# Optimization experiments

Hardware: AMD Instinct MI355X
Metric: run time of the kernel (lower is better)

Reference implementation:

```python
import jax, jax.numpy as jnp
import numpy as np

B, L, D, H = 2, 256, 256, 4
DH = D // H  # 64


def setup_inputs() -> dict:
    key = jax.random.key(0)
    ks = jax.random.split(key, 20)
    inp = {
        "q": jax.random.normal(ks[0], (B, L, D), jnp.float32),
        "k": jax.random.normal(ks[1], (B, L, D), jnp.float32),
        "v": jax.random.normal(ks[2], (B, L, D), jnp.float32),
        "attn_mask": jnp.zeros((L, L), jnp.float32),  # nonzero => masked
        "key_padding_mask": jnp.zeros((B, L), bool),
        "pitch_rel": jax.random.normal(ks[3], (B, L, L, D), jnp.float32),
        "dur_rel": jax.random.normal(ks[4], (B, L, L, D), jnp.float32),
    }
    scale = 1.0 / np.sqrt(D)
    names = ["Wq", "Wk", "Wv", "fc", "pr", "dr"]
    for i, n in enumerate(names):
        inp[n + "_w"] = jax.random.normal(ks[5 + 2 * i], (D, D), jnp.float32) * scale
        inp[n + "_b"] = jax.random.normal(ks[6 + 2 * i], (D,), jnp.float32) * 0.01
    return inp


def _linear(x, w, b):
    # torch nn.Linear: y = x @ W^T + b
    return jnp.matmul(x, w.T) + b


def reference(q, k, v, attn_mask, key_padding_mask, pitch_rel, dur_rel,
              Wq_w, Wq_b, Wk_w, Wk_b, Wv_w, Wv_b, fc_w, fc_b,
              pr_w, pr_b, dr_w, dr_b):
    Bq, Lq, Dm = q.shape
    Lk = k.shape[1]
    # project and split heads -> (B, H, L, DH)
    def heads(x, w, b):
        return _linear(x, w, b).reshape(Bq, -1, H, DH).transpose(0, 2, 1, 3)
    qh, kh, vh = heads(q, Wq_w, Wq_b), heads(k, Wk_w, Wk_b), heads(v, Wv_w, Wv_b)

    # content scores: (B, H, Lq, Lk)
    logits = jnp.einsum("bhid,bhjd->bhij", qh, kh)

    # relative pitch bias: pitch_rel (B, Lq, Lk, D) -> (B, Lq, Lk, H, DH)
    pr = _linear(pitch_rel, pr_w, pr_b).reshape(Bq, Lq, Lk, H, DH)
    logits = logits + jnp.einsum("bhid,bijhd->bhij", qh, pr)

    dr = _linear(dur_rel, dr_w, dr_b).reshape(Bq, Lq, Lk, H, DH)
    logits = logits + jnp.einsum("bhid,bijhd->bhij", qh, dr)

    logits = logits / np.sqrt(DH)

    # mask: key_padding_mask broadcast over the QUERY axis (as in source),
    # attn_mask nonzero => masked
    mask = jnp.logical_or(key_padding_mask[:, None, :, None],
                          (attn_mask != 0)[None, None, :, :])
    logits = jnp.where(mask, jnp.float32(-9e15), logits)

    attn = jax.nn.softmax(logits, axis=-1)  # (B, H, Lq, Lk)
    out = jnp.einsum("bhij,bhjd->bhid", attn, vh)  # (B, H, Lq, DH)
    out = out.transpose(0, 2, 1, 3).reshape(Bq, Lq, Dm)
    out = _linear(out, fc_w, fc_b)  # dropout is identity in eval mode
    return out, attn
```

## Files before the change

### kernel.cpp

```cpp
#include <hip/hip_runtime.h>
#include <math.h>


__global__ __launch_bounds__(256) void k_proj(
    const float* __restrict__ q, const float* __restrict__ k_, const float* __restrict__ v,
    const float* __restrict__ Wq, const float* __restrict__ Bq,
    const float* __restrict__ Wk, const float* __restrict__ Bk,
    const float* __restrict__ Wv, const float* __restrict__ Bv,
    float* __restrict__ qh, float* __restrict__ kh, float* __restrict__ vh) {
  int blk = blockIdx.x;
  int m = blk >> 5;
  int r = blk & 31;
  int b = r >> 4, it = (r >> 2) & 3, ot = r & 3;
  const float* X = (m == 0) ? q : (m == 1) ? k_ : v;
  const float* W = (m == 0) ? Wq : (m == 1) ? Wk : Wv;
  const float* Bs = (m == 0) ? Bq : (m == 1) ? Bk : Bv;
  float* OUT = (m == 0) ? qh : (m == 1) ? kh : vh;
  const float scale = (m == 0) ? 0.125f : 1.0f;

  __shared__ float xs[64][33];
  __shared__ float ws[64][33];
  int tid = threadIdx.x;
  int ti = tid >> 4, to = tid & 15;
  int lr = tid >> 2, lc = (tid & 3) * 8;
  float acc[4][4] = {};

  for (int k0 = 0; k0 < 256; k0 += 32) {
    float4 a0 = *(const float4*)(X + (size_t)(b * 256 + it * 64 + lr) * 256 + k0 + lc);
    float4 a1 = *(const float4*)(X + (size_t)(b * 256 + it * 64 + lr) * 256 + k0 + lc + 4);
    xs[lr][lc + 0] = a0.x; xs[lr][lc + 1] = a0.y; xs[lr][lc + 2] = a0.z; xs[lr][lc + 3] = a0.w;
    xs[lr][lc + 4] = a1.x; xs[lr][lc + 5] = a1.y; xs[lr][lc + 6] = a1.z; xs[lr][lc + 7] = a1.w;
    float4 w0 = *(const float4*)(W + (size_t)(ot * 64 + lr) * 256 + k0 + lc);
    float4 w1 = *(const float4*)(W + (size_t)(ot * 64 + lr) * 256 + k0 + lc + 4);
    ws[lr][lc + 0] = w0.x; ws[lr][lc + 1] = w0.y; ws[lr][lc + 2] = w0.z; ws[lr][lc + 3] = w0.w;
    ws[lr][lc + 4] = w1.x; ws[lr][lc + 5] = w1.y; ws[lr][lc + 6] = w1.z; ws[lr][lc + 7] = w1.w;
    __syncthreads();
#pragma unroll
    for (int kk = 0; kk < 32; ++kk) {
      float xv0 = xs[ti * 4 + 0][kk], xv1 = xs[ti * 4 + 1][kk];
      float xv2 = xs[ti * 4 + 2][kk], xv3 = xs[ti * 4 + 3][kk];
      float wv0 = ws[0 * 16 + to][kk], wv1 = ws[1 * 16 + to][kk];
      float wv2 = ws[2 * 16 + to][kk], wv3 = ws[3 * 16 + to][kk];
      acc[0][0] += xv0 * wv0; acc[0][1] += xv0 * wv1; acc[0][2] += xv0 * wv2; acc[0][3] += xv0 * wv3;
      acc[1][0] += xv1 * wv0; acc[1][1] += xv1 * wv1; acc[1][2] += xv1 * wv2; acc[1][3] += xv1 * wv3;
      acc[2][0] += xv2 * wv0; acc[2][1] += xv2 * wv1; acc[2][2] += xv2 * wv2; acc[2][3] += xv2 * wv3;
      acc[3][0] += xv3 * wv0; acc[3][1] += xv3 * wv1; acc[3][2] += xv3 * wv2; acc[3][3] += xv3 * wv3;
    }
    __syncthreads();
  }
#pragma unroll
  for (int ii = 0; ii < 4; ++ii)
#pragma unroll
    for (int oo = 0; oo < 4; ++oo) {
      int i = it * 64 + ti * 4 + ii;
      int dd = oo * 16 + to;
      OUT[(size_t)((b * 4 + ot) * 256 + i) * 64 + dd] = (acc[ii][oo] + Bs[ot * 64 + dd]) * scale;
    }
}

static __device__ void body_qprdr(int blk, const float* __restrict__ qh,
                                  const float* __restrict__ prw, const float* __restrict__ drw,
                                  float* __restrict__ qpr, float* __restrict__ qdr) {
  int t = blk >> 7;
  int r2 = blk & 127;
  int rt = r2 >> 2, et = r2 & 3;
  const float* W = t ? drw : prw;
  float* OUT = t ? qdr : qpr;
  int h = (rt >> 2) & 3;

  __shared__ float xs[64][33];
  __shared__ float ws2[32][64];
  int tid = threadIdx.x;
  int ti = tid >> 4, to = tid & 15;
  float acc[4][4] = {};

  for (int k0 = 0; k0 < 64; k0 += 32) {
    int lr = tid >> 2, lc = (tid & 3) * 8;
    float4 a0 = *(const float4*)(qh + (size_t)(rt * 64 + lr) * 64 + k0 + lc);
    float4 a1 = *(const float4*)(qh + (size_t)(rt * 64 + lr) * 64 + k0 + lc + 4);
    xs[lr][lc + 0] = a0.x; xs[lr][lc + 1] = a0.y; xs[lr][lc + 2] = a0.z; xs[lr][lc + 3] = a0.w;
    xs[lr][lc + 4] = a1.x; xs[lr][lc + 5] = a1.y; xs[lr][lc + 6] = a1.z; xs[lr][lc + 7] = a1.w;
    int wr = tid >> 3, wc = (tid & 7) * 8;
    float4 w0 = *(const float4*)(W + (size_t)(h * 64 + k0 + wr) * 256 + et * 64 + wc);
    float4 w1 = *(const float4*)(W + (size_t)(h * 64 + k0 + wr) * 256 + et * 64 + wc + 4);
    ws2[wr][wc + 0] = w0.x; ws2[wr][wc + 1] = w0.y; ws2[wr][wc + 2] = w0.z; ws2[wr][wc + 3] = w0.w;
    ws2[wr][wc + 4] = w1.x; ws2[wr][wc + 5] = w1.y; ws2[wr][wc + 6] = w1.z; ws2[wr][wc + 7] = w1.w;
    __syncthreads();
#pragma unroll
    for (int kk = 0; kk < 32; ++kk) {
      float xv0 = xs[ti * 4 + 0][kk], xv1 = xs[ti * 4 + 1][kk];
      float xv2 = xs[ti * 4 + 2][kk], xv3 = xs[ti * 4 + 3][kk];
      float wv0 = ws2[kk][0 * 16 + to], wv1 = ws2[kk][1 * 16 + to];
      float wv2 = ws2[kk][2 * 16 + to], wv3 = ws2[kk][3 * 16 + to];
      acc[0][0] += xv0 * wv0; acc[0][1] += xv0 * wv1; acc[0][2] += xv0 * wv2; acc[0][3] += xv0 * wv3;
      acc[1][0] += xv1 * wv0; acc[1][1] += xv1 * wv1; acc[1][2] += xv1 * wv2; acc[1][3] += xv1 * wv3;
      acc[2][0] += xv2 * wv0; acc[2][1] += xv2 * wv1; acc[2][2] += xv2 * wv2; acc[2][3] += xv2 * wv3;
      acc[3][0] += xv3 * wv0; acc[3][1] += xv3 * wv1; acc[3][2] += xv3 * wv2; acc[3][3] += xv3 * wv3;
    }
    __syncthreads();
  }
#pragma unroll
  for (int ii = 0; ii < 4; ++ii)
#pragma unroll
    for (int oo = 0; oo < 4; ++oo)
      OUT[(size_t)(rt * 64 + ti * 4 + ii) * 256 + et * 64 + oo * 16 + to] = acc[ii][oo];
}

static __device__ void body_qk(int blk, const float* __restrict__ qh,
                               const float* __restrict__ kh, float* __restrict__ qk) {
  int bh = blk >> 4, it = (blk >> 2) & 3, jt = blk & 3;
  __shared__ float xs[64][33];
  __shared__ float ys[64][33];
  int tid = threadIdx.x;
  int ti = tid >> 4, to = tid & 15;
  float acc[4][4] = {};

  for (int k0 = 0; k0 < 64; k0 += 32) {
    int lr = tid >> 2, lc = (tid & 3) * 8;
    float4 a0 = *(const float4*)(qh + (size_t)(bh * 256 + it * 64 + lr) * 64 + k0 + lc);
    float4 a1 = *(const float4*)(qh + (size_t)(bh * 256 + it * 64 + lr) * 64 + k0 + lc + 4);
    xs[lr][lc + 0] = a0.x; xs[lr][lc + 1] = a0.y; xs[lr][lc + 2] = a0.z; xs[lr][lc + 3] = a0.w;
    xs[lr][lc + 4] = a1.x; xs[lr][lc + 5] = a1.y; xs[lr][lc + 6] = a1.z; xs[lr][lc + 7] = a1.w;
    float4 b0 = *(const float4*)(kh + (size_t)(bh * 256 + jt * 64 + lr) * 64 + k0 + lc);
    float4 b1 = *(const float4*)(kh + (size_t)(bh * 256 + jt * 64 + lr) * 64 + k0 + lc + 4);
    ys[lr][lc + 0] = b0.x; ys[lr][lc + 1] = b0.y; ys[lr][lc + 2] = b0.z; ys[lr][lc + 3] = b0.w;
    ys[lr][lc + 4] = b1.x; ys[lr][lc + 5] = b1.y; ys[lr][lc + 6] = b1.z; ys[lr][lc + 7] = b1.w;
    __syncthreads();
#pragma unroll
    for (int kk = 0; kk < 32; ++kk) {
      float xv0 = xs[ti * 4 + 0][kk], xv1 = xs[ti * 4 + 1][kk];
      float xv2 = xs[ti * 4 + 2][kk], xv3 = xs[ti * 4 + 3][kk];
      float wv0 = ys[0 * 16 + to][kk], wv1 = ys[1 * 16 + to][kk];
      float wv2 = ys[2 * 16 + to][kk], wv3 = ys[3 * 16 + to][kk];
      acc[0][0] += xv0 * wv0; acc[0][1] += xv0 * wv1; acc[0][2] += xv0 * wv2; acc[0][3] += xv0 * wv3;
      acc[1][0] += xv1 * wv0; acc[1][1] += xv1 * wv1; acc[1][2] += xv1 * wv2; acc[1][3] += xv1 * wv3;
      acc[2][0] += xv2 * wv0; acc[2][1] += xv2 * wv1; acc[2][2] += xv2 * wv2; acc[2][3] += xv2 * wv3;
      acc[3][0] += xv3 * wv0; acc[3][1] += xv3 * wv1; acc[3][2] += xv3 * wv2; acc[3][3] += xv3 * wv3;
    }
    __syncthreads();
  }
#pragma unroll
  for (int ii = 0; ii < 4; ++ii)
#pragma unroll
    for (int jj = 0; jj < 4; ++jj)
      qk[(size_t)(bh * 256 + it * 64 + ti * 4 + ii) * 256 + jt * 64 + jj * 16 + to] = acc[ii][jj];
}

static __device__ void body_transpose(int blk, const float* __restrict__ in,
                                      float* __restrict__ out) {
  __shared__ float t[32][33];
  int bx = blk & 7, by = blk >> 3;
  int x = threadIdx.x & 31, y0 = threadIdx.x >> 5;
#pragma unroll
  for (int yy = 0; yy < 32; yy += 8)
    t[yy + y0][x] = in[(size_t)(by * 32 + yy + y0) * 256 + bx * 32 + x];
  __syncthreads();
#pragma unroll
  for (int yy = 0; yy < 32; yy += 8)
    out[(size_t)(bx * 32 + yy + y0) * 256 + by * 32 + x] = t[x][yy + y0];
}

__global__ __launch_bounds__(256) void k_mid(
    const float* __restrict__ qh, const float* __restrict__ kh,
    const float* __restrict__ prw, const float* __restrict__ drw,
    float* __restrict__ qpr, float* __restrict__ qdr, float* __restrict__ qk,
    const float* __restrict__ fcw, float* __restrict__ fcT) {
  int blk = blockIdx.x;
  if (blk < 256) body_qprdr(blk, qh, prw, drw, qpr, qdr);
  else if (blk < 384) body_qk(blk - 256, qh, kh, qk);
  else body_transpose(blk - 384, fcw, fcT);
}

__global__ __launch_bounds__(256, 8) void k_bias(
    const float* __restrict__ pitch, const float* __restrict__ dur,
    const float* __restrict__ qpr, const float* __restrict__ qdr,
    float* __restrict__ bias) {
  int blk = blockIdx.x;
  int jc = blk & 3;
  int bi = blk >> 2;
  int b = bi >> 8, i = bi & 255;
  int tid = threadIdx.x, w = tid >> 6, l = tid & 63;
  int j0 = jc * 64 + w * 16;

  __shared__ float red[4][4][4][65];

  float4 qp[4], qd[4];
#pragma unroll
  for (int h = 0; h < 4; ++h) {
    qp[h] = *(const float4*)(qpr + (size_t)((b * 4 + h) * 256 + i) * 256 + 4 * l);
    qd[h] = *(const float4*)(qdr + (size_t)((b * 4 + h) * 256 + i) * 256 + 4 * l);
  }

  int p2 = l & 15, row_o = p2 >> 2, h_o = p2 & 3, sub = l >> 4;
  size_t obase = ((size_t)(b * 4 + h_o) * 256 + i) * 256 + j0 + row_o;

  const float* pbase = pitch + ((size_t)bi * 256 + j0) * 256 + 4 * l;
  const float* dbase = dur + ((size_t)bi * 256 + j0) * 256 + 4 * l;

#pragma unroll
  for (int g = 0; g < 4; ++g) {
#pragma unroll
    for (int r = 0; r < 4; ++r) {
      float4 P = *(const float4*)(pbase + (g * 4 + r) * 256);
      float4 Dv = *(const float4*)(dbase + (g * 4 + r) * 256);
      red[w][r][0][l] = P.x * qp[0].x + P.y * qp[0].y + P.z * qp[0].z + P.w * qp[0].w
                      + Dv.x * qd[0].x + Dv.y * qd[0].y + Dv.z * qd[0].z + Dv.w * qd[0].w;
      red[w][r][1][l] = P.x * qp[1].x + P.y * qp[1].y + P.z * qp[1].z + P.w * qp[1].w
                      + Dv.x * qd[1].x + Dv.y * qd[1].y + Dv.z * qd[1].z + Dv.w * qd[1].w;
      red[w][r][2][l] = P.x * qp[2].x + P.y * qp[2].y + P.z * qp[2].z + P.w * qp[2].w
                      + Dv.x * qd[2].x + Dv.y * qd[2].y + Dv.z * qd[2].z + Dv.w * qd[2].w;
      red[w][r][3][l] = P.x * qp[3].x + P.y * qp[3].y + P.z * qp[3].z + P.w * qp[3].w
                      + Dv.x * qd[3].x + Dv.y * qd[3].y + Dv.z * qd[3].z + Dv.w * qd[3].w;
    }
    float x = 0.f;
    {
      const float* rr = &red[w][row_o][h_o][sub * 16];
#pragma unroll
      for (int c = 0; c < 16; ++c) x += rr[c];
    }
    x += __shfl_xor(x, 16);
    x += __shfl_xor(x, 32);
    if (l < 16) bias[obase + g * 4] = x;
  }
}

__global__ __launch_bounds__(256) void k_pvfc(
    const float* __restrict__ bias, const float* __restrict__ amask,
    const unsigned char* __restrict__ kpm, const float* __restrict__ vh,
    const float* __restrict__ fcT, const float* __restrict__ fcb,
    float* __restrict__ attn, float* __restrict__ out) {
  int b = blockIdx.x >> 8, i = blockIdx.x & 255;
  int tid = threadIdx.x;
  int h = tid >> 6, l = tid & 63;

  __shared__ float arow[4][256];
  __shared__ float pre[256];

  bool rowm = kpm[b * 256 + i] != 0;
  float* qrow = attn + (size_t)((b * 4 + h) * 256 + i) * 256;
  const float* brow = bias + (size_t)((b * 4 + h) * 256 + i) * 256;
  float4 v4 = *(float4*)(qrow + 4 * l);
  float4 b4 = *(const float4*)(brow + 4 * l);
  float4 m4 = *(const float4*)(amask + (size_t)i * 256 + 4 * l);
  float v0 = (rowm || m4.x != 0.f) ? -9e15f : v4.x + b4.x;
  float v1 = (rowm || m4.y != 0.f) ? -9e15f : v4.y + b4.y;
  float v2 = (rowm || m4.z != 0.f) ? -9e15f : v4.z + b4.z;
  float v3 = (rowm || m4.w != 0.f) ? -9e15f : v4.w + b4.w;

  float mx = fmaxf(fmaxf(v0, v1), fmaxf(v2, v3));
#pragma unroll
  for (int m = 1; m <= 32; m <<= 1) mx = fmaxf(mx, __shfl_xor(mx, m));
  float e0 = __expf(v0 - mx), e1 = __expf(v1 - mx);
  float e2 = __expf(v2 - mx), e3 = __expf(v3 - mx);
  float sm = e0 + e1 + e2 + e3;
#pragma unroll
  for (int m = 1; m <= 32; m <<= 1) sm += __shfl_xor(sm, m);
  float inv = 1.0f / sm;
  float4 a4 = make_float4(e0 * inv, e1 * inv, e2 * inv, e3 * inv);
  *(float4*)(qrow + 4 * l) = a4;
  *(float4*)&arow[h][4 * l] = a4;

  float acc = 0.f;
  const float* vbase = vh + (size_t)(b * 4 + h) * 256 * 64 + l;
#pragma unroll 4
  for (int jj = 0; jj < 256; ++jj) acc += arow[h][jj] * vbase[(size_t)jj * 64];
  pre[tid] = acc;
  __syncthreads();

  float acc2 = fcb[tid];
#pragma unroll 4
  for (int c = 0; c < 256; ++c) acc2 += pre[c] * fcT[(size_t)c * 256 + tid];
  out[(size_t)(b * 256 + i) * 256 + tid] = acc2;
}

extern "C" void kernel_launch(void* const* d_in, const int* in_sizes, int n_in,
                              void* d_out, int out_size, void* d_ws, size_t ws_size,
                              hipStream_t stream) {
  (void)in_sizes; (void)n_in; (void)out_size; (void)ws_size;
  const float* q = (const float*)d_in[0];
  const float* k = (const float*)d_in[1];
  const float* v = (const float*)d_in[2];
  const float* amask = (const float*)d_in[3];
  const unsigned char* kpm = (const unsigned char*)d_in[4];
  const float* pitch = (const float*)d_in[5];
  const float* dur = (const float*)d_in[6];
  const float* Wq = (const float*)d_in[7];
  const float* Bq = (const float*)d_in[8];
  const float* Wk = (const float*)d_in[9];
  const float* Bk = (const float*)d_in[10];
  const float* Wv = (const float*)d_in[11];
  const float* Bv = (const float*)d_in[12];
  const float* fcw = (const float*)d_in[13];
  const float* fcb = (const float*)d_in[14];
  const float* prw = (const float*)d_in[15];
  const float* drw = (const float*)d_in[17];

  float* out = (float*)d_out;
  float* attn = out + 2 * 256 * 256;

  float* wsf = (float*)d_ws;
  float* qh = wsf;
  float* kh = qh + 131072;
  float* vh = kh + 131072;
  float* qpr = vh + 131072;
  float* qdr = qpr + 524288;
  float* fcT = qdr + 524288;
  float* bias = fcT + 65536;

  k_proj<<<96, 256, 0, stream>>>(q, k, v, Wq, Bq, Wk, Bk, Wv, Bv, qh, kh, vh);
  k_mid<<<448, 256, 0, stream>>>(qh, kh, prw, drw, qpr, qdr, attn, fcw, fcT);
  k_bias<<<2048, 256, 0, stream>>>(pitch, dur, qpr, qdr, bias);
  k_pvfc<<<512, 256, 0, stream>>>(bias, amask, kpm, vh, fcT, fcb, attn, out);
}
```

Baseline: 114.5 us.

## Double-buffer streaming loads in k_bias with inline asm nontemporal loads

Result: no change. 114.0 us (-0.4%).

```diff
diff --git a/kernel.cpp b/kernel.cpp
--- a/kernel.cpp
+++ b/kernel.cpp
@@ -1,6 +1,18 @@
 #include <hip/hip_runtime.h>
 #include <math.h>
 
+
+typedef float f4v __attribute__((ext_vector_type(4)));
+
+#define SLD(dst, ptr)                                                     \
+  asm volatile("global_load_dwordx4 %0, %1, off sc0 sc1 nt"               \
+               : "=v"(dst)                                                \
+               : "v"((unsigned long long)(const void*)(ptr))              \
+               : "memory")
+
+#define VW(n)                                             \
+  asm volatile("s_waitcnt vmcnt(%0)" ::"i"(n) : "memory"); \
+  __builtin_amdgcn_sched_barrier(0)
 
 __global__ __launch_bounds__(256) void k_proj(
     const float* __restrict__ q, const float* __restrict__ k_, const float* __restrict__ v,
@@ -171,7 +183,7 @@
   else body_transpose(blk - 384, fcw, fcT);
 }
 
-__global__ __launch_bounds__(256, 8) void k_bias(
+__global__ __launch_bounds__(256, 4) void k_bias(
     const float* __restrict__ pitch, const float* __restrict__ dur,
     const float* __restrict__ qpr, const float* __restrict__ qdr,
     float* __restrict__ bias) {
@@ -197,31 +209,58 @@
   const float* pbase = pitch + ((size_t)bi * 256 + j0) * 256 + 4 * l;
   const float* dbase = dur + ((size_t)bi * 256 + j0) * 256 + 4 * l;
 
-#pragma unroll
-  for (int g = 0; g < 4; ++g) {
-#pragma unroll
-    for (int r = 0; r < 4; ++r) {
-      float4 P = *(const float4*)(pbase + (g * 4 + r) * 256);
-      float4 Dv = *(const float4*)(dbase + (g * 4 + r) * 256);
-      red[w][r][0][l] = P.x * qp[0].x + P.y * qp[0].y + P.z * qp[0].z + P.w * qp[0].w
-                      + Dv.x * qd[0].x + Dv.y * qd[0].y + Dv.z * qd[0].z + Dv.w * qd[0].w;
-      red[w][r][1][l] = P.x * qp[1].x + P.y * qp[1].y + P.z * qp[1].z + P.w * qp[1].w
-                      + Dv.x * qd[1].x + Dv.y * qd[1].y + Dv.z * qd[1].z + Dv.w * qd[1].w;
-      red[w][r][2][l] = P.x * qp[2].x + P.y * qp[2].y + P.z * qp[2].z + P.w * qp[2].w
-                      + Dv.x * qd[2].x + Dv.y * qd[2].y + Dv.z * qd[2].z + Dv.w * qd[2].w;
-      red[w][r][3][l] = P.x * qp[3].x + P.y * qp[3].y + P.z * qp[3].z + P.w * qp[3].w
-                      + Dv.x * qd[3].x + Dv.y * qd[3].y + Dv.z * qd[3].z + Dv.w * qd[3].w;
-    }
-    float x = 0.f;
-    {
-      const float* rr = &red[w][row_o][h_o][sub * 16];
-#pragma unroll
-      for (int c = 0; c < 16; ++c) x += rr[c];
-    }
-    x += __shfl_xor(x, 16);
-    x += __shfl_xor(x, 32);
-    if (l < 16) bias[obase + g * 4] = x;
-  }
+  asm volatile("s_waitcnt vmcnt(0)" ::: "memory");
+
+  f4v PA[4], DA[4], PB[4], DB[4];
+
+#define ISSUE(PP, DD, g)                                  \
+  {                                                       \
+    _Pragma("unroll") for (int r = 0; r < 4; ++r) {       \
+      SLD(PP[r], pbase + ((g) * 4 + r) * 256);            \
+      SLD(DD[r], dbase + ((g) * 4 + r) * 256);            \
+    }                                                     \
+  }
+
+#define COMPUTE(PP, DD, g)                                                        \
+  {                                                                               \
+    _Pragma("unroll") for (int r = 0; r < 4; ++r) {                               \
+      red[w][r][0][l] = PP[r].x * qp[0].x + PP[r].y * qp[0].y + PP[r].z * qp[0].z \
+                      + PP[r].w * qp[0].w + DD[r].x * qd[0].x + DD[r].y * qd[0].y \
+                      + DD[r].z * qd[0].z + DD[r].w * qd[0].w;                    \
+      red[w][r][1][l] = PP[r].x * qp[1].x + PP[r].y * qp[1].y + PP[r].z * qp[1].z \
+                      + PP[r].w * qp[1].w + DD[r].x * qd[1].x + DD[r].y * qd[1].y \
+                      + DD[r].z * qd[1].z + DD[r].w * qd[1].w;                    \
+      red[w][r][2][l] = PP[r].x * qp[2].x + PP[r].y * qp[2].y + PP[r].z * qp[2].z \
+                      + PP[r].w * qp[2].w + DD[r].x * qd[2].x + DD[r].y * qd[2].y \
+                      + DD[r].z * qd[2].z + DD[r].w * qd[2].w;                    \
+      red[w][r][3][l] = PP[r].x * qp[3].x + PP[r].y * qp[3].y + PP[r].z * qp[3].z \
+                      + PP[r].w * qp[3].w + DD[r].x * qd[3].x + DD[r].y * qd[3].y \
+                      + DD[r].z * qd[3].z + DD[r].w * qd[3].w;                    \
+    }                                                                             \
+    float x = 0.f;                                                                \
+    {                                                                             \
+      const float* rr = &red[w][row_o][h_o][sub * 16];                            \
+      _Pragma("unroll") for (int c = 0; c < 16; ++c) x += rr[c];                  \
+    }                                                                             \
+    x += __shfl_xor(x, 16);                                                       \
+    x += __shfl_xor(x, 32);                                                       \
+    if (l < 16) bias[obase + (g) * 4] = x;                                        \
+  }
+
+  ISSUE(PA, DA, 0);
+  ISSUE(PB, DB, 1);
+  VW(8);
+  COMPUTE(PA, DA, 0);
+  ISSUE(PA, DA, 2);
+  VW(8);
+  COMPUTE(PB, DB, 1);
+  ISSUE(PB, DB, 3);
+  VW(8);
+  COMPUTE(PA, DA, 2);
+  VW(0);
+  COMPUTE(PB, DB, 3);
+#undef ISSUE
+#undef COMPUTE
 }
 
 __global__ __launch_bounds__(256) void k_pvfc(
```
